# Kernel tuning notes

Measured on AMD Instinct MI355X. Metric: run time of the kernel, lower is better.

## Reference

```python
import jax, jax.numpy as jnp
import numpy as np

BS, IC, L = 8, 64, 32768
OC, K = 64, 3
STRIDE, PAD, DIL = 1, 1, 1
ALPHA = 0.5  # SmoothQuant scaling_factor
QMAX = 127.0  # symmetric int8 fake quant


def fake_quant(t):
    # per-tensor symmetric int8 fake quantization with straight-through estimator
    amax = jnp.max(jnp.abs(jax.lax.stop_gradient(t)))
    s = jnp.where(amax == 0, 1.0, amax / QMAX)
    q = jnp.clip(jnp.round(t / s), -QMAX, QMAX) * s
    return t + jax.lax.stop_gradient(q - t)


def setup_inputs() -> dict:
    key = jax.random.key(0)
    k1, k2, k3 = jax.random.split(key, 3)
    x = jax.random.normal(k1, (BS, IC, L), dtype=jnp.float32)
    weight = jax.random.normal(k2, (OC, IC, K), dtype=jnp.float32) * 0.05
    bias = jax.random.normal(k3, (OC,), dtype=jnp.float32) * 0.01
    return {"x": x, "weight": weight, "bias": bias}


def reference(x, weight, bias):
    bs, ic, length = x.shape
    out_len = (length + 2 * PAD - DIL * (K - 1) - 1) // STRIDE + 1
    # im2col / unfold: (bs, ic, K, out_len) with F.unfold's channel-major, kernel-pos-minor order
    xp = jnp.pad(x, ((0, 0), (0, 0), (PAD, PAD)))
    patches = jnp.stack(
        [xp[:, :, j * DIL : j * DIL + STRIDE * (out_len - 1) + 1 : STRIDE] for j in range(K)],
        axis=2,
    )  # (bs, ic, K, out_len)
    cols = patches.reshape(bs, ic * K, out_len).transpose(0, 2, 1).reshape(bs * out_len, ic * K)
    w = weight.reshape(OC, ic * K)
    # dynamic SmoothQuant scales (detached in original)
    w_scale = jnp.max(jnp.abs(jax.lax.stop_gradient(w)), axis=0)        # (ic*K,)
    act_scale = jnp.max(jnp.abs(jax.lax.stop_gradient(cols)), axis=0)   # (ic*K,)
    scale = act_scale ** ALPHA / w_scale ** (1.0 - ALPHA)
    scale = jnp.where(scale == 0, 1.0, scale)
    xq = fake_quant(cols / scale)
    wq = fake_quant(w * scale)
    out = xq @ wq.T  # (bs*out_len, OC)
    out = out.reshape(bs, out_len, OC).transpose(0, 2, 1) + bias[None, :, None]
    return out
```

## Files before the change

kernel.cpp:

```cpp
#include <hip/hip_runtime.h>

#define L_LEN 32768
#define QMAXF 127.0f
#define TPB 4

typedef __attribute__((ext_vector_type(4))) int v4i;


__global__ __launch_bounds__(1024) void actamax_kernel(const float* __restrict__ x,
                                                       float* __restrict__ wsf) {
    const int ic = blockIdx.x, b = blockIdx.y;
    const float4* row = (const float4*)(x + ((size_t)(b*64 + ic) << 15));
    float mA = 0.0f, mNF = 0.0f, mNL = 0.0f;
    #pragma unroll
    for (int i = 0; i < 8; ++i) {
        int f = threadIdx.x + (i << 10);
        float4 v = row[f];
        float ax = fabsf(v.x), ay = fabsf(v.y), az = fabsf(v.z), aw = fabsf(v.w);
        float m4 = fmaxf(fmaxf(ax, ay), fmaxf(az, aw));
        mA = fmaxf(mA, m4);
        if (f == 0) {
            mNF = fmaxf(mNF, fmaxf(ay, fmaxf(az, aw)));
            mNL = fmaxf(mNL, m4);
        } else if (f == 8191) {
            mNF = fmaxf(mNF, m4);
            mNL = fmaxf(mNL, fmaxf(ax, fmaxf(ay, az)));
        } else {
            mNF = fmaxf(mNF, m4);
            mNL = fmaxf(mNL, m4);
        }
    }
    #pragma unroll
    for (int off = 32; off; off >>= 1) {
        mA  = fmaxf(mA,  __shfl_down(mA,  off));
        mNF = fmaxf(mNF, __shfl_down(mNF, off));
        mNL = fmaxf(mNL, __shfl_down(mNL, off));
    }
    __shared__ float red[3][16];
    int wid = threadIdx.x >> 6;
    if ((threadIdx.x & 63) == 0) { red[0][wid] = mA; red[1][wid] = mNF; red[2][wid] = mNL; }
    __syncthreads();
    if (threadIdx.x == 0) {
        mA = red[0][0]; mNF = red[1][0]; mNL = red[2][0];
        #pragma unroll
        for (int i = 1; i < 16; ++i) {
            mA  = fmaxf(mA,  red[0][i]);
            mNF = fmaxf(mNF, red[1][i]);
            mNL = fmaxf(mNL, red[2][i]);
        }
        float* p = wsf + (ic*8 + b)*3;
        p[0] = mNL; p[1] = mA; p[2] = mNF;
    }
}

__global__ __launch_bounds__(256) void fused_conv_kernel(const float* __restrict__ x,
                                                         const float* __restrict__ w,
                                                         const float* __restrict__ bias,
                                                         const float* __restrict__ wsf,
                                                         float* __restrict__ out) {
    __shared__ int   bsm[3072];
    __shared__ float scl[192];
    __shared__ float red[256];
    __shared__ float bias_s[64];

    const int tid  = threadIdx.x;
    const int b    = blockIdx.y;
    const int lane = tid & 63;
    const int wv   = tid >> 6;

    float ax = 0.0f, aww = 0.0f;
    if (tid < 192) {
        float wsc = 0.0f;
        #pragma unroll 8
        for (int o = 0; o < 64; ++o) wsc = fmaxf(wsc, fabsf(w[o*192 + tid]));
        int ic = tid / 3, k = tid - ic*3;
        float asc = 0.0f;
        #pragma unroll
        for (int bb = 0; bb < 8; ++bb) asc = fmaxf(asc, wsf[(ic*8 + bb)*3 + k]);
        float sc = sqrtf(asc) / sqrtf(wsc);
        if (sc == 0.0f) sc = 1.0f;
        scl[tid] = sc;
        ax  = asc / sc;
        aww = wsc * sc;
    }
    if (tid < 64) bias_s[tid] = bias[tid];
    red[tid] = ax; __syncthreads();
    for (int s = 128; s; s >>= 1) { if (tid < s) red[tid] = fmaxf(red[tid], red[tid+s]); __syncthreads(); }
    float axm = red[0]; __syncthreads();
    red[tid] = aww; __syncthreads();
    for (int s = 128; s; s >>= 1) { if (tid < s) red[tid] = fmaxf(red[tid], red[tid+s]); __syncthreads(); }
    float awm = red[0];
    const float s_x = (axm == 0.0f) ? 1.0f : axm / QMAXF;
    const float s_w = (awm == 0.0f) ? 1.0f : awm / QMAXF;
    const float sxw = s_x * s_w;

    for (int idx = tid; idx < 3072; idx += 256) {
        int oc = idx / 48, dwi = idx - oc*48, j0 = dwi*4;
        unsigned pk = 0;
        #pragma unroll
        for (int bb = 0; bb < 4; ++bb) {
            int j = j0 + bb;
            float q = rintf((w[oc*192 + j] * scl[j]) / s_w);
            q = fminf(fmaxf(q, -QMAXF), QMAXF);
            pk |= (((unsigned)(int)q) & 255u) << (8*bb);
        }
        int mt = oc >> 4, m = oc & 15, c = j0 >> 4, s = c >> 2, kq = c & 3;
        bsm[((mt*3 + s)*64 + kq*16 + m)*4 + ((j0 & 15) >> 2)] = (int)pk;
    }
    __syncthreads();
    v4i afrag[12];
    const v4i* bsmv = (const v4i*)bsm;
    #pragma unroll
    for (int i = 0; i < 12; ++i) afrag[i] = bsmv[i*64 + lane];

    const int tq  = tid & 15;
    const int icg = tid >> 4;
    const int tb  = tq << 2;

    float rv[12];
    #pragma unroll
    for (int jj = 0; jj < 12; ++jj) rv[jj] = 1.0f / (scl[icg*12 + jj] * s_x);

    float xv[4][6];
    {
        const int t0 = (blockIdx.x * TPB) << 6;
        #pragma unroll
        for (int ici = 0; ici < 4; ++ici) {
            const float* rowp = x + (((size_t)(b*64 + icg*4 + ici)) << 15) + t0 + tb;
            float4 mid = *(const float4*)rowp;
            float lm = (t0 + tb > 0)           ? rowp[-1] : 0.0f;
            float rp = (t0 + tb + 4 < L_LEN)   ? rowp[4]  : 0.0f;
            xv[ici][0] = lm;    xv[ici][1] = mid.x; xv[ici][2] = mid.y;
            xv[ici][3] = mid.z; xv[ici][4] = mid.w; xv[ici][5] = rp;
        }
    }

    for (int it = 0; it < TPB; ++it) {
        const int t0c = (blockIdx.x * TPB + it) << 6;

        unsigned pkq[12];
        #pragma unroll
        for (int dt = 0; dt < 4; ++dt) {
            #pragma unroll
            for (int dw = 0; dw < 3; ++dw) {
                unsigned pk = 0;
                #pragma unroll
                for (int bb = 0; bb < 4; ++bb) {
                    int jloc = dw*4 + bb;
                    int ici = jloc / 3, k = jloc - ici*3;
                    float q = rintf(xv[ici][dt + k] * rv[jloc]);
                    q = fminf(fmaxf(q, -QMAXF), QMAXF);
                    pk |= (((unsigned)(int)q) & 255u) << (8*bb);
                }
                pkq[dt*3 + dw] = pk;
            }
        }

        __syncthreads();
        #pragma unroll
        for (int dt = 0; dt < 4; ++dt) {
            int t = tb + dt, wt = t >> 4, n = t & 15;
            #pragma unroll
            for (int dw = 0; dw < 3; ++dw) {
                int j0 = icg*12 + dw*4;
                int c = j0 >> 4, s = c >> 2, kq = c & 3;
                bsm[((wt*3 + s)*64 + kq*16 + n)*4 + ((j0 & 15) >> 2)] = (int)pkq[dt*3 + dw];
            }
        }
        __syncthreads();

        if (it + 1 < TPB) {
            const int t0n = (blockIdx.x * TPB + it + 1) << 6;
            #pragma unroll
            for (int ici = 0; ici < 4; ++ici) {
                const float* rowp = x + (((size_t)(b*64 + icg*4 + ici)) << 15) + t0n + tb;
                float4 mid = *(const float4*)rowp;
                float lm = (t0n + tb > 0)          ? rowp[-1] : 0.0f;
                float rp = (t0n + tb + 4 < L_LEN)  ? rowp[4]  : 0.0f;
                xv[ici][0] = lm;    xv[ici][1] = mid.x; xv[ici][2] = mid.y;
                xv[ici][3] = mid.z; xv[ici][4] = mid.w; xv[ici][5] = rp;
            }
        }

        v4i acc[4];
        #pragma unroll
        for (int mt = 0; mt < 4; ++mt) acc[mt] = (v4i){0,0,0,0};
        const v4i* bsmv2 = (const v4i*)bsm;
        #pragma unroll
        for (int s = 0; s < 3; ++s) {
            v4i bf = bsmv2[(wv*3 + s)*64 + lane];
            #pragma unroll
            for (int mt = 0; mt < 4; ++mt)
                acc[mt] = __builtin_amdgcn_mfma_i32_16x16x64_i8(afrag[mt*3 + s], bf, acc[mt], 0, 0, 0);
        }

        const int tg   = t0c + (wv << 4) + (lane & 15);
        const int rowq = (lane >> 4) << 2;
        #pragma unroll
        for (int mt = 0; mt < 4; ++mt) {
            #pragma unroll
            for (int i = 0; i < 4; ++i) {
                int oc = mt*16 + rowq + i;
                out[(((size_t)(b*64 + oc)) << 15) + tg] = (float)acc[mt][i] * sxw + bias_s[oc];
            }
        }
    }
}

extern "C" void kernel_launch(void* const* d_in, const int* in_sizes, int n_in,
                              void* d_out, int out_size, void* d_ws, size_t ws_size,
                              hipStream_t stream) {
    const float* x    = (const float*)d_in[0];
    const float* w    = (const float*)d_in[1];
    const float* bias = (const float*)d_in[2];
    float* out = (float*)d_out;
    float* wsf = (float*)d_ws;

    hipLaunchKernelGGL(actamax_kernel,   dim3(64, 8),  dim3(1024), 0, stream, x, wsf);
    hipLaunchKernelGGL(fused_conv_kernel, dim3(512 / TPB, 8), dim3(256), 0, stream,
                       x, w, bias, wsf, out);
}
```

Before: 165.1 us.

## Move scale and weight quantization into a single-block prep kernel, swizzle LDS

Weight abs-max, SmoothQuant scales, the global scale reductions and int8 weight packing were redone in every conv block. They are now computed once by a new single-block prep kernel and written to workspace, and the conv blocks only load the packed A fragments and reciprocal scales. The B-tile stores and loads in LDS also get an XOR swizzle to cut bank conflicts. This adds a third kernel launch and a serial one-block step between the two main kernels.

```diff
diff --git a/kernel.cpp b/kernel.cpp
--- a/kernel.cpp
+++ b/kernel.cpp
@@ -53,22 +53,13 @@
     }
 }
 
-__global__ __launch_bounds__(256) void fused_conv_kernel(const float* __restrict__ x,
-                                                         const float* __restrict__ w,
-                                                         const float* __restrict__ bias,
-                                                         const float* __restrict__ wsf,
-                                                         float* __restrict__ out) {
-    __shared__ int   bsm[3072];
+__global__ __launch_bounds__(256) void prep_kernel(const float* __restrict__ w,
+                                                   float* __restrict__ wsf,
+                                                   unsigned int* __restrict__ wsa) {
     __shared__ float scl[192];
     __shared__ float red[256];
-    __shared__ float bias_s[64];
-
-    const int tid  = threadIdx.x;
-    const int b    = blockIdx.y;
-    const int lane = tid & 63;
-    const int wv   = tid >> 6;
-
-    float ax = 0.0f, aww = 0.0f;
+    const int tid = threadIdx.x;
+    float ax = 0.0f, aw = 0.0f;
     if (tid < 192) {
         float wsc = 0.0f;
         #pragma unroll 8
@@ -76,24 +67,24 @@
         int ic = tid / 3, k = tid - ic*3;
         float asc = 0.0f;
         #pragma unroll
-        for (int bb = 0; bb < 8; ++bb) asc = fmaxf(asc, wsf[(ic*8 + bb)*3 + k]);
+        for (int b = 0; b < 8; ++b) asc = fmaxf(asc, wsf[(ic*8 + b)*3 + k]);
         float sc = sqrtf(asc) / sqrtf(wsc);
         if (sc == 0.0f) sc = 1.0f;
         scl[tid] = sc;
-        ax  = asc / sc;
-        aww = wsc * sc;
-    }
-    if (tid < 64) bias_s[tid] = bias[tid];
+        ax = asc / sc;
+        aw = wsc * sc;
+    }
     red[tid] = ax; __syncthreads();
     for (int s = 128; s; s >>= 1) { if (tid < s) red[tid] = fmaxf(red[tid], red[tid+s]); __syncthreads(); }
     float axm = red[0]; __syncthreads();
-    red[tid] = aww; __syncthreads();
+    red[tid] = aw; __syncthreads();
     for (int s = 128; s; s >>= 1) { if (tid < s) red[tid] = fmaxf(red[tid], red[tid+s]); __syncthreads(); }
     float awm = red[0];
-    const float s_x = (axm == 0.0f) ? 1.0f : axm / QMAXF;
-    const float s_w = (awm == 0.0f) ? 1.0f : awm / QMAXF;
-    const float sxw = s_x * s_w;
-
+    float s_x = (axm == 0.0f) ? 1.0f : axm / QMAXF;
+    float s_w = (awm == 0.0f) ? 1.0f : awm / QMAXF;
+    if (tid < 192) wsf[1536 + tid] = 1.0f / (scl[tid] * s_x);
+    if (tid == 0)  wsf[1728] = s_x * s_w;
+    __syncthreads();
     for (int idx = tid; idx < 3072; idx += 256) {
         int oc = idx / 48, dwi = idx - oc*48, j0 = dwi*4;
         unsigned pk = 0;
@@ -105,21 +96,24 @@
             pk |= (((unsigned)(int)q) & 255u) << (8*bb);
         }
         int mt = oc >> 4, m = oc & 15, c = j0 >> 4, s = c >> 2, kq = c & 3;
-        bsm[((mt*3 + s)*64 + kq*16 + m)*4 + ((j0 & 15) >> 2)] = (int)pk;
-    }
-    __syncthreads();
-    v4i afrag[12];
-    const v4i* bsmv = (const v4i*)bsm;
-    #pragma unroll
-    for (int i = 0; i < 12; ++i) afrag[i] = bsmv[i*64 + lane];
+        wsa[((mt*3 + s)*64 + kq*16 + m)*4 + ((j0 & 15) >> 2)] = pk;
+    }
+}
+
+__global__ __launch_bounds__(256) void conv_mfma_kernel(const float* __restrict__ x,
+                                                        const float* __restrict__ bias,
+                                                        const float* __restrict__ wsf,
+                                                        const v4i* __restrict__ wsa,
+                                                        float* __restrict__ out) {
+    __shared__ int bsm[3072];
+    const int tid  = threadIdx.x;
+    const int b    = blockIdx.y;
+    const int lane = tid & 63;
+    const int wv   = tid >> 6;
 
     const int tq  = tid & 15;
     const int icg = tid >> 4;
     const int tb  = tq << 2;
-
-    float rv[12];
-    #pragma unroll
-    for (int jj = 0; jj < 12; ++jj) rv[jj] = 1.0f / (scl[icg*12 + jj] * s_x);
 
     float xv[4][6];
     {
@@ -134,6 +128,15 @@
             xv[ici][3] = mid.z; xv[ici][4] = mid.w; xv[ici][5] = rp;
         }
     }
+
+    v4i afrag[12];
+    #pragma unroll
+    for (int i = 0; i < 12; ++i) afrag[i] = wsa[i*64 + lane];
+
+    float rv[12];
+    #pragma unroll
+    for (int jj = 0; jj < 12; ++jj) rv[jj] = wsf[1536 + icg*12 + jj];
+    const float sxw = wsf[1728];
 
     for (int it = 0; it < TPB; ++it) {
         const int t0c = (blockIdx.x * TPB + it) << 6;
@@ -156,7 +159,7 @@
             }
         }
 
-        __syncthreads();
+        if (it) __syncthreads();
         #pragma unroll
         for (int dt = 0; dt < 4; ++dt) {
             int t = tb + dt, wt = t >> 4, n = t & 15;
@@ -164,7 +167,9 @@
             for (int dw = 0; dw < 3; ++dw) {
                 int j0 = icg*12 + dw*4;
                 int c = j0 >> 4, s = c >> 2, kq = c & 3;
-                bsm[((wt*3 + s)*64 + kq*16 + n)*4 + ((j0 & 15) >> 2)] = (int)pkq[dt*3 + dw];
+                int G = (wt*3 + s)*64 + kq*16 + n;
+                G ^= (G >> 6) & 7;
+                bsm[G*4 + ((j0 & 15) >> 2)] = (int)pkq[dt*3 + dw];
             }
         }
         __syncthreads();
@@ -185,10 +190,12 @@
         v4i acc[4];
         #pragma unroll
         for (int mt = 0; mt < 4; ++mt) acc[mt] = (v4i){0,0,0,0};
-        const v4i* bsmv2 = (const v4i*)bsm;
+        const v4i* bsmv = (const v4i*)bsm;
         #pragma unroll
         for (int s = 0; s < 3; ++s) {
-            v4i bf = bsmv2[(wv*3 + s)*64 + lane];
+            int Gr = (wv*3 + s)*64 + lane;
+            Gr ^= (wv*3 + s) & 7;
+            v4i bf = bsmv[Gr];
             #pragma unroll
             for (int mt = 0; mt < 4; ++mt)
                 acc[mt] = __builtin_amdgcn_mfma_i32_16x16x64_i8(afrag[mt*3 + s], bf, acc[mt], 0, 0, 0);
@@ -201,7 +208,7 @@
             #pragma unroll
             for (int i = 0; i < 4; ++i) {
                 int oc = mt*16 + rowq + i;
-                out[(((size_t)(b*64 + oc)) << 15) + tg] = (float)acc[mt][i] * sxw + bias_s[oc];
+                out[(((size_t)(b*64 + oc)) << 15) + tg] = (float)acc[mt][i] * sxw + bias[oc];
             }
         }
     }
@@ -215,8 +222,10 @@
     const float* bias = (const float*)d_in[2];
     float* out = (float*)d_out;
     float* wsf = (float*)d_ws;
-
-    hipLaunchKernelGGL(actamax_kernel,   dim3(64, 8),  dim3(1024), 0, stream, x, wsf);
-    hipLaunchKernelGGL(fused_conv_kernel, dim3(512 / TPB, 8), dim3(256), 0, stream,
-                       x, w, bias, wsf, out);
-}
+    unsigned int* wsa = (unsigned int*)((char*)d_ws + 8192);
+
+    hipLaunchKernelGGL(actamax_kernel,   dim3(64, 8),       dim3(1024), 0, stream, x, wsf);
+    hipLaunchKernelGGL(prep_kernel,      dim3(1),           dim3(256),  0, stream, w, wsf, wsa);
+    hipLaunchKernelGGL(conv_mfma_kernel, dim3(512/TPB, 8),  dim3(256),  0, stream,
+                       x, bias, wsf, (const v4i*)wsa, out);
+}
```

Measured after the change: 150.5 us. -8.8%, faster.
